# Kernel optimization log

Measured on AMD Instinct MI355X. Metric: run time of the kernel, lower is better.

## Reference

```python
import jax, jax.numpy as jnp
import numpy as np

B, T, D_IN, D, K = 16, 1024, 768, 512, 8192


def setup_inputs() -> dict:
    key = jax.random.key(0)
    k1, k2, k3 = jax.random.split(key, 3)
    x = jax.random.normal(k1, (B, T, D_IN), dtype=jnp.float32)
    W_proj = jax.random.normal(k2, (D_IN, D), dtype=jnp.float32) * (1.0 / np.sqrt(D_IN))
    b_proj = jnp.zeros((D,), dtype=jnp.float32)
    # uniform(-1/K, 1/K) matches the torch init
    codebook = jax.random.uniform(k3, (K, D), dtype=jnp.float32, minval=-1.0 / K, maxval=1.0 / K)
    return {"x": x, "W_proj": W_proj, "b_proj": b_proj, "codebook": codebook}


def reference(x, W_proj, b_proj, codebook):
    commitment_cost = 0.25
    inputs = jnp.einsum('btf,fd->btd', x, W_proj) + b_proj          # [B,T,D]
    flat = inputs.reshape(-1, D)                                    # [N,D]
    # squared-euclidean distances to every codeword: [N,K]
    dists = (jnp.sum(flat * flat, axis=1, keepdims=True)
             + jnp.sum(codebook * codebook, axis=1)
             - 2.0 * flat @ codebook.T)
    idx = jnp.argmin(dists, axis=1)                                 # [N] int
    quantized_flat = codebook[idx]                                  # gather == one_hot @ codebook
    quantized = quantized_flat.reshape(B, T, D)

    commitment_loss = jnp.mean((jax.lax.stop_gradient(quantized) - inputs) ** 2)
    codebook_loss = jnp.mean((quantized - jax.lax.stop_gradient(inputs)) ** 2)
    vq_loss = codebook_loss + commitment_cost * commitment_loss

    # straight-through estimator
    quantized_st = inputs + jax.lax.stop_gradient(quantized - inputs)

    # perplexity from mean one-hot occupancy
    N = flat.shape[0]
    counts = jnp.zeros((K,), dtype=jnp.float32).at[idx].add(1.0)
    avg_probs = counts / N
    perplexity = jnp.exp(-jnp.sum(avg_probs * jnp.log(avg_probs + 1e-10)))

    tokens = idx.reshape(B, T)
    return quantized_st, tokens, vq_loss, perplexity
```

## Files before the change

### kernel.cpp

```cpp
#include <hip/hip_runtime.h>
#include <math.h>

#define NROW 16384
#define DIN  768
#define DD   512
#define KCB  8192
#define NBLK 64
#define QELEMS 8388608
#define TOK_OFF 8388608
#define LOSS_OFF 8404992
#define PERP_OFF 8404993

typedef unsigned long long ull;

__device__ inline unsigned int fsort(float s) {
    unsigned int u = __float_as_uint(s);
    return (u & 0x80000000u) ? ~u : (u | 0x80000000u);
}

__device__ inline float leaf128_sq(const float* __restrict__ p) {
    float m[16];
    #pragma unroll
    for (int l = 0; l < 16; l++) {
        float j0 = __fmul_rn(p[l +   0], p[l +   0]);
        float j1 = __fmul_rn(p[l +  16], p[l +  16]);
        float j2 = __fmul_rn(p[l +  32], p[l +  32]);
        float j3 = __fmul_rn(p[l +  48], p[l +  48]);
        float j4 = __fmul_rn(p[l +  64], p[l +  64]);
        float j5 = __fmul_rn(p[l +  80], p[l +  80]);
        float j6 = __fmul_rn(p[l +  96], p[l +  96]);
        float j7 = __fmul_rn(p[l + 112], p[l + 112]);
        m[l] = __fadd_rn(__fadd_rn(__fadd_rn(j0, j1), __fadd_rn(j2, j3)),
                         __fadd_rn(__fadd_rn(j4, j5), __fadd_rn(j6, j7)));
    }
    #pragma unroll
    for (int s = 8; s >= 1; s >>= 1)
        #pragma unroll
        for (int l = 0; l < 8; l++)
            if (l < s) m[l] = __fadd_rn(m[l], m[l + s]);
    return m[0];
}
__device__ inline float np_sum512_sq(const float* __restrict__ v) {
    float L0 = leaf128_sq(v);
    float L1 = leaf128_sq(v + 128);
    float L2 = leaf128_sq(v + 256);
    float L3 = leaf128_sq(v + 384);
    return __fadd_rn(__fadd_rn(L0, L1), __fadd_rn(L2, L3));
}

__global__ __launch_bounds__(256) void femu_kernel(const float* __restrict__ X, const float* __restrict__ W,
                                                   const float* __restrict__ Bv, float* __restrict__ F) {
    __shared__ float xs[64][68];
    __shared__ float wsh[64][132];
    const int tid = threadIdx.x;
    const int n0 = blockIdx.y * 64, j0 = blockIdx.x * 128;
    const int nt = tid >> 4, jt = tid & 15;
    float acc[4][8];
    #pragma unroll
    for (int i = 0; i < 4; i++)
        #pragma unroll
        for (int q = 0; q < 8; q++) acc[i][q] = 0.0f;

    for (int fc = 0; fc < DIN; fc += 64) {
        #pragma unroll
        for (int k = 0; k < 4; k++) {
            int e = tid * 4 + k;
            int r = e >> 4, c4 = (e & 15) * 4;
            *(float4*)&xs[r][c4] = *(const float4*)(X + (size_t)(n0 + r) * DIN + fc + c4);
        }
        #pragma unroll
        for (int k = 0; k < 8; k++) {
            int e = tid * 8 + k;
            int r = e >> 5, c4 = (e & 31) * 4;
            *(float4*)&wsh[r][c4] = *(const float4*)(W + (size_t)(fc + r) * DD + j0 + c4);
        }
        __syncthreads();
        for (int f = 0; f < 64; f++) {
            float xv[4], wv[8];
            #pragma unroll
            for (int i = 0; i < 4; i++) xv[i] = xs[nt * 4 + i][f];
            #pragma unroll
            for (int q = 0; q < 8; q++) wv[q] = wsh[f][jt * 8 + q];
            #pragma unroll
            for (int i = 0; i < 4; i++)
                #pragma unroll
                for (int q = 0; q < 8; q++)
                    acc[i][q] = __fadd_rn(acc[i][q], __fmul_rn(xv[i], wv[q]));
        }
        __syncthreads();
    }
    #pragma unroll
    for (int i = 0; i < 4; i++)
        #pragma unroll
        for (int q = 0; q < 8; q++) {
            int n = n0 + nt * 4 + i, j = j0 + jt * 8 + q;
            F[(size_t)n * DD + j] = __fadd_rn(acc[i][q], Bv[j]);
        }
}

__global__ __launch_bounds__(256) void norms_kernel(const float* __restrict__ F, const float* __restrict__ CB,
                                                    float* __restrict__ Av, float* __restrict__ Bn) {
    int t = blockIdx.x * 256 + threadIdx.x;
    if (t < NROW) {
        Av[t] = np_sum512_sq(F + (size_t)t * DD);
    } else {
        int k = t - NROW;
        if (k < KCB) Bn[k] = np_sum512_sq(CB + (size_t)k * DD);
    }
}

__global__ __launch_bounds__(256) void score_kernel(const float* __restrict__ F, const float* __restrict__ CB,
                                                    const float* __restrict__ Av, const float* __restrict__ Bn,
                                                    ull* __restrict__ keys) {
    __shared__ float At[16][132];
    __shared__ float Bt[16][132];
    const int tid = threadIdx.x;
    const int tr = tid >> 4, tc = tid & 15;
    const int m0 = blockIdx.y * 128, n0 = blockIdx.x * 128;
    float acc[8][8] = {};
    for (int kt = 0; kt < DD; kt += 16) {
        #pragma unroll
        for (int i = 0; i < 2; i++) {
            int c = tid + i * 256;
            int row = c >> 2, kc = (c & 3) * 4;
            float4 v = *(const float4*)(F + (size_t)(m0 + row) * DD + kt + kc);
            At[kc + 0][row] = v.x; At[kc + 1][row] = v.y; At[kc + 2][row] = v.z; At[kc + 3][row] = v.w;
        }
        #pragma unroll
        for (int i = 0; i < 2; i++) {
            int c = tid + i * 256;
            int row = c >> 2, kc = (c & 3) * 4;
            float4 v = *(const float4*)(CB + (size_t)(n0 + row) * DD + kt + kc);
            Bt[kc + 0][row] = v.x; Bt[kc + 1][row] = v.y; Bt[kc + 2][row] = v.z; Bt[kc + 3][row] = v.w;
        }
        __syncthreads();
        #pragma unroll
        for (int kk = 0; kk < 16; kk++) {
            float4 a0 = *(float4*)&At[kk][tr * 8];
            float4 a1 = *(float4*)&At[kk][tr * 8 + 4];
            float4 b0 = *(float4*)&Bt[kk][tc * 8];
            float4 b1 = *(float4*)&Bt[kk][tc * 8 + 4];
            float a[8] = {a0.x, a0.y, a0.z, a0.w, a1.x, a1.y, a1.z, a1.w};
            float b[8] = {b0.x, b0.y, b0.z, b0.w, b1.x, b1.y, b1.z, b1.w};
            #pragma unroll
            for (int i = 0; i < 8; i++)
                #pragma unroll
                for (int j = 0; j < 8; j++)
                    acc[i][j] = fmaf(a[i], b[j], acc[i][j]);
        }
        __syncthreads();
    }
    float Bk[8];
    #pragma unroll
    for (int j = 0; j < 8; j++) Bk[j] = Bn[n0 + tc * 8 + j];
    #pragma unroll
    for (int i = 0; i < 8; i++) {
        int row = m0 + tr * 8 + i;
        float Ai = Av[row];
        ull mk = ~0ull;
        #pragma unroll
        for (int j = 0; j < 8; j++) {
            float t1 = __fadd_rn(Ai, Bk[j]);
            float t2 = __fsub_rn(t1, __fmul_rn(2.0f, acc[i][j]));
            ull key = ((ull)fsort(t2) << 32) | (unsigned int)(n0 + tc * 8 + j);
            mk = mk < key ? mk : key;
        }
        #pragma unroll
        for (int off = 1; off < 16; off <<= 1) {
            ull o = __shfl_xor(mk, off, 16);
            mk = mk < o ? mk : o;
        }
        if (tc == 0) keys[(size_t)row * NBLK + blockIdx.x] = mk;
    }
}

__global__ __launch_bounds__(256) void reduce_kernel(const ull* __restrict__ keys, int* __restrict__ tokens) {
    int w = threadIdx.x >> 6, lane = threadIdx.x & 63;
    int row = blockIdx.x * 4 + w;
    ull mk = keys[(size_t)row * NBLK + lane];
    #pragma unroll
    for (int off = 1; off < 64; off <<= 1) {
        ull o = __shfl_xor(mk, off, 64);
        mk = mk < o ? mk : o;
    }
    if (lane == 0) tokens[row] = (int)(mk & 0xFFFFFFFFull);
}

__global__ __launch_bounds__(256) void epilogue_kernel(const float* __restrict__ CB, const int* __restrict__ tokens,
                                                       unsigned int* __restrict__ counts, float* __restrict__ lossp,
                                                       float* out) {
    int w = threadIdx.x >> 6, lane = threadIdx.x & 63;
    int row = blockIdx.x * 4 + w;
    int idx = tokens[row];
    const float4* c4 = (const float4*)(CB + (size_t)idx * DD);
    float4* q4 = (float4*)(out + (size_t)row * DD);
    float4 c0 = c4[lane], c1 = c4[lane + 64];
    float4 f0 = q4[lane], f1 = q4[lane + 64];
    float s = (c0.x - f0.x) * (c0.x - f0.x) + (c0.y - f0.y) * (c0.y - f0.y)
            + (c0.z - f0.z) * (c0.z - f0.z) + (c0.w - f0.w) * (c0.w - f0.w)
            + (c1.x - f1.x) * (c1.x - f1.x) + (c1.y - f1.y) * (c1.y - f1.y)
            + (c1.z - f1.z) * (c1.z - f1.z) + (c1.w - f1.w) * (c1.w - f1.w);
    q4[lane] = c0;
    q4[lane + 64] = c1;
    #pragma unroll
    for (int off = 32; off; off >>= 1) s += __shfl_xor(s, off, 64);
    if (lane == 0) {
        atomicAdd(lossp, s);
        atomicAdd(&counts[idx], 1u);
        out[TOK_OFF + row] = (float)idx;
    }
}

__global__ __launch_bounds__(256) void finalize_kernel(const unsigned int* __restrict__ counts,
                                                       const float* __restrict__ lossp, float* out) {
    __shared__ double red[256];
    int t = threadIdx.x;
    double h = 0.0;
    for (int n = t; n < KCB; n += 256) {
        unsigned int c = counts[n];
        if (c) {
            double p = (double)c / (double)NROW;
            h += p * log(p + 1e-10);
        }
    }
    red[t] = h;
    __syncthreads();
    for (int off = 128; off; off >>= 1) {
        if (t < off) red[t] += red[t + off];
        __syncthreads();
    }
    if (t == 0) {
        out[LOSS_OFF] = (float)(1.25 * ((double)lossp[0] / (double)QELEMS));
        out[PERP_OFF] = (float)exp(-red[0]);
    }
}

extern "C" void kernel_launch(void* const* d_in, const int* in_sizes, int n_in,
                              void* d_out, int out_size, void* d_ws, size_t ws_size,
                              hipStream_t stream) {
    const float* X  = (const float*)d_in[0];
    const float* W  = (const float*)d_in[1];
    const float* Bv = (const float*)d_in[2];
    const float* CB = (const float*)d_in[3];
    float* out = (float*)d_out;
    float* F = out;

    char* ws = (char*)d_ws;
    ull* keys = (ull*)ws;
    int* tokens = (int*)(keys + (size_t)NROW * NBLK);
    unsigned int* counts = (unsigned int*)(tokens + NROW);
    float* lossp = (float*)(counts + KCB);
    float* Aemu = lossp + 1;
    float* Bemu = Aemu + NROW;

    size_t off_zero = (char*)counts - ws;
    hipMemsetAsync(ws + off_zero, 0, KCB * 4 + 4, stream);

    femu_kernel<<<dim3(DD / 128, NROW / 64), 256, 0, stream>>>(X, W, Bv, F);
    norms_kernel<<<(NROW + KCB) / 256, 256, 0, stream>>>(F, CB, Aemu, Bemu);
    score_kernel<<<dim3(NBLK, NROW / 128), 256, 0, stream>>>(F, CB, Aemu, Bemu, keys);
    reduce_kernel<<<NROW / 4, 256, 0, stream>>>(keys, tokens);
    epilogue_kernel<<<NROW / 4, 256, 0, stream>>>(CB, tokens, counts, lossp, out);
    finalize_kernel<<<1, 256, 0, stream>>>(counts, lossp, out);
}
```

Measured before the change: 2.072 ms.

## Enlarge register tiles in projection and distance GEMMs for more reuse

The projection GEMM moves from a 64x128 tile with a 64-deep K chunk to a 128x128 tile with 8x8 per-thread outputs and a transposed X tile in shared memory. Stores become float4 with interleaved column mapping. The distance GEMM grows to 256x128 tiles with 16x8 accumulators per thread and launch bounds of two blocks. The aim is to cut shared-memory and global-load traffic per FMA, at the cost of more register pressure and fewer blocks in the grid.

```diff
diff --git a/kernel.cpp b/kernel.cpp
--- a/kernel.cpp
+++ b/kernel.cpp
@@ -50,39 +50,42 @@
 
 __global__ __launch_bounds__(256) void femu_kernel(const float* __restrict__ X, const float* __restrict__ W,
                                                    const float* __restrict__ Bv, float* __restrict__ F) {
-    __shared__ float xs[64][68];
-    __shared__ float wsh[64][132];
+    __shared__ float xsT[16][132];
+    __shared__ float wsh[16][132];
     const int tid = threadIdx.x;
-    const int n0 = blockIdx.y * 64, j0 = blockIdx.x * 128;
     const int nt = tid >> 4, jt = tid & 15;
-    float acc[4][8];
-    #pragma unroll
-    for (int i = 0; i < 4; i++)
+    const int n0 = blockIdx.y * 128, j0 = blockIdx.x * 128;
+    float acc[8][8];
+    #pragma unroll
+    for (int i = 0; i < 8; i++)
         #pragma unroll
         for (int q = 0; q < 8; q++) acc[i][q] = 0.0f;
 
-    for (int fc = 0; fc < DIN; fc += 64) {
-        #pragma unroll
-        for (int k = 0; k < 4; k++) {
-            int e = tid * 4 + k;
-            int r = e >> 4, c4 = (e & 15) * 4;
-            *(float4*)&xs[r][c4] = *(const float4*)(X + (size_t)(n0 + r) * DIN + fc + c4);
-        }
-        #pragma unroll
-        for (int k = 0; k < 8; k++) {
-            int e = tid * 8 + k;
-            int r = e >> 5, c4 = (e & 31) * 4;
+    for (int fc = 0; fc < DIN; fc += 16) {
+        #pragma unroll
+        for (int i = 0; i < 2; i++) {
+            int idx = tid + i * 256;
+            int row = idx >> 2, kc = (idx & 3) * 4;
+            float4 v = *(const float4*)(X + (size_t)(n0 + row) * DIN + fc + kc);
+            xsT[kc + 0][row] = v.x; xsT[kc + 1][row] = v.y; xsT[kc + 2][row] = v.z; xsT[kc + 3][row] = v.w;
+        }
+        #pragma unroll
+        for (int i = 0; i < 2; i++) {
+            int idx = tid + i * 256;
+            int r = idx >> 5, c4 = (idx & 31) * 4;
             *(float4*)&wsh[r][c4] = *(const float4*)(W + (size_t)(fc + r) * DD + j0 + c4);
         }
         __syncthreads();
-        for (int f = 0; f < 64; f++) {
-            float xv[4], wv[8];
+        #pragma unroll 4
+        for (int f = 0; f < 16; f++) {
+            float4 x0 = *(float4*)&xsT[f][nt * 8];
+            float4 x1 = *(float4*)&xsT[f][nt * 8 + 4];
+            float4 w0 = *(float4*)&wsh[f][jt * 4];
+            float4 w1 = *(float4*)&wsh[f][64 + jt * 4];
+            float xv[8] = {x0.x, x0.y, x0.z, x0.w, x1.x, x1.y, x1.z, x1.w};
+            float wv[8] = {w0.x, w0.y, w0.z, w0.w, w1.x, w1.y, w1.z, w1.w};
             #pragma unroll
-            for (int i = 0; i < 4; i++) xv[i] = xs[nt * 4 + i][f];
-            #pragma unroll
-            for (int q = 0; q < 8; q++) wv[q] = wsh[f][jt * 8 + q];
-            #pragma unroll
-            for (int i = 0; i < 4; i++)
+            for (int i = 0; i < 8; i++)
                 #pragma unroll
                 for (int q = 0; q < 8; q++)
                     acc[i][q] = __fadd_rn(acc[i][q], __fmul_rn(xv[i], wv[q]));
@@ -90,12 +93,19 @@
         __syncthreads();
     }
     #pragma unroll
-    for (int i = 0; i < 4; i++)
-        #pragma unroll
-        for (int q = 0; q < 8; q++) {
-            int n = n0 + nt * 4 + i, j = j0 + jt * 8 + q;
-            F[(size_t)n * DD + j] = __fadd_rn(acc[i][q], Bv[j]);
-        }
+    for (int i = 0; i < 8; i++) {
+        int n = n0 + nt * 8 + i;
+        #pragma unroll
+        for (int h = 0; h < 2; h++) {
+            int col = j0 + h * 64 + jt * 4;
+            float4 o;
+            o.x = __fadd_rn(acc[i][h * 4 + 0], Bv[col + 0]);
+            o.y = __fadd_rn(acc[i][h * 4 + 1], Bv[col + 1]);
+            o.z = __fadd_rn(acc[i][h * 4 + 2], Bv[col + 2]);
+            o.w = __fadd_rn(acc[i][h * 4 + 3], Bv[col + 3]);
+            *(float4*)(F + (size_t)n * DD + col) = o;
+        }
+    }
 }
 
 __global__ __launch_bounds__(256) void norms_kernel(const float* __restrict__ F, const float* __restrict__ CB,
@@ -109,41 +119,49 @@
     }
 }
 
-__global__ __launch_bounds__(256) void score_kernel(const float* __restrict__ F, const float* __restrict__ CB,
-                                                    const float* __restrict__ Av, const float* __restrict__ Bn,
-                                                    ull* __restrict__ keys) {
-    __shared__ float At[16][132];
+__global__ __launch_bounds__(256, 2) void score_kernel(const float* __restrict__ F, const float* __restrict__ CB,
+                                                       const float* __restrict__ Av, const float* __restrict__ Bn,
+                                                       ull* __restrict__ keys) {
+    __shared__ float At[16][260];
     __shared__ float Bt[16][132];
     const int tid = threadIdx.x;
     const int tr = tid >> 4, tc = tid & 15;
-    const int m0 = blockIdx.y * 128, n0 = blockIdx.x * 128;
-    float acc[8][8] = {};
+    const int m0 = blockIdx.y * 256, n0 = blockIdx.x * 128;
+    float acc[16][8];
+    #pragma unroll
+    for (int i = 0; i < 16; i++)
+        #pragma unroll
+        for (int j = 0; j < 8; j++) acc[i][j] = 0.0f;
+
     for (int kt = 0; kt < DD; kt += 16) {
         #pragma unroll
-        for (int i = 0; i < 2; i++) {
-            int c = tid + i * 256;
-            int row = c >> 2, kc = (c & 3) * 4;
+        for (int i = 0; i < 4; i++) {
+            int idx = tid + i * 256;
+            int row = idx >> 2, kc = (idx & 3) * 4;
             float4 v = *(const float4*)(F + (size_t)(m0 + row) * DD + kt + kc);
             At[kc + 0][row] = v.x; At[kc + 1][row] = v.y; At[kc + 2][row] = v.z; At[kc + 3][row] = v.w;
         }
         #pragma unroll
         for (int i = 0; i < 2; i++) {
-            int c = tid + i * 256;
-            int row = c >> 2, kc = (c & 3) * 4;
-            float4 v = *(const float4*)(CB + (size_t)(n0 + row) * DD + kt + kc);
-            Bt[kc + 0][row] = v.x; Bt[kc + 1][row] = v.y; Bt[kc + 2][row] = v.z; Bt[kc + 3][row] = v.w;
-        }
-        __syncthreads();
-        #pragma unroll
+            int idx = tid + i * 256;
+            int col = idx >> 2, kc = (idx & 3) * 4;
+            float4 v = *(const float4*)(CB + (size_t)(n0 + col) * DD + kt + kc);
+            Bt[kc + 0][col] = v.x; Bt[kc + 1][col] = v.y; Bt[kc + 2][col] = v.z; Bt[kc + 3][col] = v.w;
+        }
+        __syncthreads();
+        #pragma unroll 4
         for (int kk = 0; kk < 16; kk++) {
-            float4 a0 = *(float4*)&At[kk][tr * 8];
-            float4 a1 = *(float4*)&At[kk][tr * 8 + 4];
-            float4 b0 = *(float4*)&Bt[kk][tc * 8];
-            float4 b1 = *(float4*)&Bt[kk][tc * 8 + 4];
-            float a[8] = {a0.x, a0.y, a0.z, a0.w, a1.x, a1.y, a1.z, a1.w};
+            float4 a0 = *(float4*)&At[kk][tr * 16];
+            float4 a1 = *(float4*)&At[kk][tr * 16 + 4];
+            float4 a2 = *(float4*)&At[kk][tr * 16 + 8];
+            float4 a3 = *(float4*)&At[kk][tr * 16 + 12];
+            float4 b0 = *(float4*)&Bt[kk][tc * 4];
+            float4 b1 = *(float4*)&Bt[kk][64 + tc * 4];
+            float a[16] = {a0.x, a0.y, a0.z, a0.w, a1.x, a1.y, a1.z, a1.w,
+                           a2.x, a2.y, a2.z, a2.w, a3.x, a3.y, a3.z, a3.w};
             float b[8] = {b0.x, b0.y, b0.z, b0.w, b1.x, b1.y, b1.z, b1.w};
             #pragma unroll
-            for (int i = 0; i < 8; i++)
+            for (int i = 0; i < 16; i++)
                 #pragma unroll
                 for (int j = 0; j < 8; j++)
                     acc[i][j] = fmaf(a[i], b[j], acc[i][j]);
@@ -151,18 +169,22 @@
         __syncthreads();
     }
     float Bk[8];
-    #pragma unroll
-    for (int j = 0; j < 8; j++) Bk[j] = Bn[n0 + tc * 8 + j];
-    #pragma unroll
-    for (int i = 0; i < 8; i++) {
-        int row = m0 + tr * 8 + i;
+    int cols[8];
+    #pragma unroll
+    for (int j = 0; j < 8; j++) {
+        cols[j] = n0 + (j < 4 ? tc * 4 + j : 64 + tc * 4 + (j - 4));
+        Bk[j] = Bn[cols[j]];
+    }
+    #pragma unroll
+    for (int i = 0; i < 16; i++) {
+        int row = m0 + tr * 16 + i;
         float Ai = Av[row];
         ull mk = ~0ull;
         #pragma unroll
         for (int j = 0; j < 8; j++) {
             float t1 = __fadd_rn(Ai, Bk[j]);
             float t2 = __fsub_rn(t1, __fmul_rn(2.0f, acc[i][j]));
-            ull key = ((ull)fsort(t2) << 32) | (unsigned int)(n0 + tc * 8 + j);
+            ull key = ((ull)fsort(t2) << 32) | (unsigned int)cols[j];
             mk = mk < key ? mk : key;
         }
         #pragma unroll
@@ -256,9 +278,9 @@
     size_t off_zero = (char*)counts - ws;
     hipMemsetAsync(ws + off_zero, 0, KCB * 4 + 4, stream);
 
-    femu_kernel<<<dim3(DD / 128, NROW / 64), 256, 0, stream>>>(X, W, Bv, F);
+    femu_kernel<<<dim3(DD / 128, NROW / 128), 256, 0, stream>>>(X, W, Bv, F);
     norms_kernel<<<(NROW + KCB) / 256, 256, 0, stream>>>(F, CB, Aemu, Bemu);
-    score_kernel<<<dim3(NBLK, NROW / 128), 256, 0, stream>>>(F, CB, Aemu, Bemu, keys);
+    score_kernel<<<dim3(NBLK, NROW / 256), 256, 0, stream>>>(F, CB, Aemu, Bemu, keys);
     reduce_kernel<<<NROW / 4, 256, 0, stream>>>(keys, tokens);
     epilogue_kernel<<<NROW / 4, 256, 0, stream>>>(CB, tokens, counts, lossp, out);
     finalize_kernel<<<1, 256, 0, stream>>>(counts, lossp, out);
```

After: 2.147 ms. 1.04x slower.
